# Kernel optimization log

Hardware: AMD Instinct MI355X
Metric: run time of the kernel (lower is better)

Reference implementation:

```python
import jax, jax.numpy as jnp
import numpy as np

TOP_K = 2

def setup_inputs() -> dict:
    key = jax.random.key(0)
    k1, k2, k3, k4 = jax.random.split(key, 4)
    T, H, I, E = 8192, 2048, 4096, 8
    s = 0.02
    return {
        "hidden_states": jax.random.normal(k1, (T, H), dtype=jnp.float32),
        "router_w": jax.random.normal(k2, (E, H), dtype=jnp.float32) * s,
        "ws": jax.random.normal(k3, (E, 2 * I, H), dtype=jnp.float32) * s,  # [gate; up]
        "w2s": jax.random.normal(k4, (E, H, I), dtype=jnp.float32) * s,
    }

def reference(hidden_states, router_w, ws, w2s):
    # Router gating: softmax over experts, top-k, NO renormalization
    logits = hidden_states @ router_w.T              # [T, E]
    probs = jax.nn.softmax(logits, axis=-1)
    topv, topi = jax.lax.top_k(probs, TOP_K)         # [T, K]
    T, E = probs.shape
    I = w2s.shape[2]
    # Dense routing-weight matrix [T, E]; top_k indices are unique per token
    w = jnp.zeros_like(probs).at[jnp.arange(T)[:, None], topi].set(topv)
    out = jnp.zeros_like(hidden_states)
    for e in range(E):  # fixed small expert loop; avoids [T,E,2I] blowup
        gate = hidden_states @ ws[e, :I].T           # [T, I]
        up = hidden_states @ ws[e, I:].T             # [T, I]
        h = jax.nn.silu(gate) * up                   # SwiGLU
        out = out + w[:, e:e + 1] * (h @ w2s[e].T)   # combine
    return out
```

## Files before the change

### kernel.cpp

```cpp
#include <hip/hip_runtime.h>
#include <cstdint>
#include <cstddef>

#define T_TOK 8192
#define HDIM  2048
#define IDIM  4096
#define NEXP  8
#define MAXT  72

typedef __bf16 bf16x8 __attribute__((ext_vector_type(8)));
typedef float  f32x4  __attribute__((ext_vector_type(4)));

#define BARRIER() __builtin_amdgcn_s_barrier()
#define LGKM0()   do { asm volatile("s_waitcnt lgkmcnt(0)" ::: "memory"); __builtin_amdgcn_sched_barrier(0); } while (0)
#define VMW(n)    do { asm volatile("s_waitcnt vmcnt(" #n ")" ::: "memory"); } while (0)
#define PRIO1()   __builtin_amdgcn_s_setprio(1)
#define PRIO0()   __builtin_amdgcn_s_setprio(0)

__device__ __forceinline__ unsigned short f2bf(float f) {
    union { float f; unsigned u; } v; v.f = f;
    unsigned r = v.u + 0x7FFFu + ((v.u >> 16) & 1u);
    return (unsigned short)(r >> 16);
}

__device__ __forceinline__ void gload16(const void* g, void* l) {
    __builtin_amdgcn_global_load_lds((__attribute__((address_space(1))) void*)g,
                                     (__attribute__((address_space(3))) void*)l,
                                     16, 0, 0);
}

__global__ __launch_bounds__(256) void router_k(const float* __restrict__ hs,
                                                const float* __restrict__ rw,
                                                float* __restrict__ wgt,
                                                int* __restrict__ counts,
                                                int* __restrict__ lists) {
    int gid  = blockIdx.x * 256 + threadIdx.x;
    int tok  = gid >> 6;
    int lane = threadIdx.x & 63;
    const float* x = hs + (size_t)tok * HDIM;

    float acc[NEXP];
#pragma unroll
    for (int e = 0; e < NEXP; ++e) acc[e] = 0.f;
    for (int h = lane; h < HDIM; h += 64) {
        float xv = x[h];
#pragma unroll
        for (int e = 0; e < NEXP; ++e) acc[e] = fmaf(xv, rw[e * HDIM + h], acc[e]);
    }
#pragma unroll
    for (int off = 32; off > 0; off >>= 1) {
#pragma unroll
        for (int e = 0; e < NEXP; ++e) acc[e] += __shfl_xor(acc[e], off, 64);
    }
    if (lane == 0) {
        float m = acc[0];
#pragma unroll
        for (int e = 1; e < NEXP; ++e) m = fmaxf(m, acc[e]);
        float p[NEXP]; float s = 0.f;
#pragma unroll
        for (int e = 0; e < NEXP; ++e) { p[e] = expf(acc[e] - m); s += p[e]; }
        float inv = 1.f / s;
        int i1 = 0;
#pragma unroll
        for (int e = 1; e < NEXP; ++e) if (acc[e] > acc[i1]) i1 = e;
        int i2 = -1;
#pragma unroll
        for (int e = 0; e < NEXP; ++e) if (e != i1 && (i2 < 0 || acc[e] > acc[i2])) i2 = e;
#pragma unroll
        for (int e = 0; e < NEXP; ++e)
            wgt[(size_t)tok * NEXP + e] = (e == i1 || e == i2) ? p[e] * inv : 0.f;
        int p1 = atomicAdd(&counts[i1], 1);
        lists[i1 * T_TOK + p1] = tok;
        int p2 = atomicAdd(&counts[i2], 1);
        lists[i2 * T_TOK + p2] = (1 << 16) | tok;
    }
}

__global__ void plan_k(const int* __restrict__ counts, int* __restrict__ offs,
                       int* __restrict__ desc, int* __restrict__ ntiles) {
    if (threadIdx.x == 0 && blockIdx.x == 0) {
        int off = 0, n = 0;
        for (int e = 0; e < NEXP; ++e) {
            offs[e] = off;
            int nt = (counts[e] + 255) >> 8;
            for (int t = 0; t < nt; ++t) desc[n++] = (e << 16) | t;
            off += nt * 256;
        }
        *ntiles = n;
    }
}

__global__ __launch_bounds__(256) void cvt_k(const float* __restrict__ in,
                                             unsigned short* __restrict__ out, long n4) {
    long i      = (long)blockIdx.x * 256 + threadIdx.x;
    long stride = (long)gridDim.x * 256;
    const float4* in4 = (const float4*)in;
    ushort4* out4 = (ushort4*)out;
    for (long j = i; j < n4; j += stride) {
        float4 v = in4[j];
        ushort4 o;
        o.x = f2bf(v.x); o.y = f2bf(v.y); o.z = f2bf(v.z); o.w = f2bf(v.w);
        out4[j] = o;
    }
}

__global__ __launch_bounds__(512, 2) void gemm1_k(const unsigned short* __restrict__ A,
                                                  const unsigned short* __restrict__ Wall,
                                                  unsigned short* __restrict__ Hout,
                                                  const int* __restrict__ lists,
                                                  const int* __restrict__ counts,
                                                  const int* __restrict__ offs,
                                                  const int* __restrict__ desc,
                                                  const int* __restrict__ ntiles) {
    const int slot = blockIdx.y;
    if (slot >= *ntiles) return;
    const int dsc = desc[slot];
    const int e = dsc >> 16, tt = dsc & 0xFFFF;
    const int cnt = counts[e];
    const int t0 = tt * 256;
    const int* list = lists + e * T_TOK;
    const unsigned short* W = Wall + (size_t)e * 2 * IDIM * HDIM;
    const int hbase = offs[e];
    const int n0 = blockIdx.x * 128;

    extern __shared__ __align__(16) char lds[];

    const int tid  = threadIdx.x;
    const int lane = tid & 63;
    const int wid  = tid >> 6;
    const int wr   = wid >> 2;
    const int wc   = wid & 3;

    const int prow = tid >> 3;
    const int pcol = (tid & 7) * 16;
    const int lcol = (pcol ^ ((prow & 7) << 4)) >> 1;
    unsigned aoff[4];
#pragma unroll
    for (int i = 0; i < 4; ++i) {
        int g = t0 + i * 64 + prow;
        int tok = list[(g < cnt) ? g : t0] & 0xFFFF;
        aoff[i] = (unsigned)tok * HDIM + lcol;
    }
    unsigned goff[2], uoff[2];
#pragma unroll
    for (int i = 0; i < 2; ++i) {
        goff[i] = (unsigned)(n0 + i * 64 + prow) * HDIM + lcol;
        uoff[i] = (unsigned)(IDIM + n0 + i * 64 + prow) * HDIM + lcol;
    }
    const int dst = tid * 16;

#define SG_AH0(b, t) do { unsigned k0_ = (unsigned)((t) & 31) * 64;      \
    gload16(A + aoff[0] + k0_, lds + (b) * 32768 + dst);                 \
    gload16(A + aoff[1] + k0_, lds + (b) * 32768 + 8192 + dst); } while (0)
#define SG_AH1(b, t) do { unsigned k0_ = (unsigned)((t) & 31) * 64;      \
    gload16(A + aoff[2] + k0_, lds + (b) * 32768 + 16384 + dst);         \
    gload16(A + aoff[3] + k0_, lds + (b) * 32768 + 24576 + dst); } while (0)
#define SG_G(b, t) do { unsigned k0_ = (unsigned)((t) & 31) * 64;        \
    gload16(W + goff[0] + k0_, lds + 65536 + (b) * 16384 + dst);         \
    gload16(W + goff[1] + k0_, lds + 65536 + (b) * 16384 + 8192 + dst); } while (0)
#define SG_U(b, t) do { unsigned k0_ = (unsigned)((t) & 31) * 64;        \
    gload16(W + uoff[0] + k0_, lds + 98304 + (b) * 16384 + dst);         \
    gload16(W + uoff[1] + k0_, lds + 98304 + (b) * 16384 + 8192 + dst); } while (0)

    const int frd = (lane & 7) << 4;
    const int cb0 = (((lane >> 4) * 16)     ) ^ frd;
    const int cb1 = (((lane >> 4) * 16) | 64) ^ frd;
    const int arow = (wr * 64 + (lane & 15)) * 128;
    const int brow = (wc * 32 + (lane & 15)) * 128;

    f32x4 accg[8][2], accu[8][2];
#pragma unroll
    for (int mi = 0; mi < 8; ++mi)
#pragma unroll
        for (int ni = 0; ni < 2; ++ni) {
            accg[mi][ni] = (f32x4){0.f, 0.f, 0.f, 0.f};
            accu[mi][ni] = (f32x4){0.f, 0.f, 0.f, 0.f};
        }

    SG_AH0(0, 0); SG_G(0, 0); SG_U(0, 0); SG_AH1(0, 0);
    SG_AH0(1, 1); SG_G(1, 1);
    VMW(0);
    BARRIER();

    const int NT = HDIM / 64;
    for (int kt = 0; kt < NT; ++kt) {
        const int b  = kt & 1;
        const int bn = b ^ 1;
        const char* la = lds + b * 32768 + arow;
        const char* lg = lds + 65536 + b * 16384 + brow;
        const char* lu = lds + 98304 + b * 16384 + brow;
        bf16x8 a0[2][4], bg[2][2], bu[2][2];

#pragma unroll
        for (int mi = 0; mi < 4; ++mi) {
            a0[0][mi] = *(const bf16x8*)(la + mi * 2048 + cb0);
            a0[1][mi] = *(const bf16x8*)(la + mi * 2048 + cb1);
        }
#pragma unroll
        for (int ni = 0; ni < 2; ++ni) {
            bg[0][ni] = *(const bf16x8*)(lg + ni * 2048 + cb0);
            bg[1][ni] = *(const bf16x8*)(lg + ni * 2048 + cb1);
        }
        SG_AH1(bn, kt + 1);
        BARRIER(); LGKM0(); PRIO1();
#pragma unroll
        for (int ks = 0; ks < 2; ++ks)
#pragma unroll
            for (int mi = 0; mi < 4; ++mi)
#pragma unroll
                for (int ni = 0; ni < 2; ++ni)
                    accg[mi][ni] = __builtin_amdgcn_mfma_f32_16x16x32_bf16(a0[ks][mi], bg[ks][ni], accg[mi][ni], 0, 0, 0);
        PRIO0();
        VMW(6);
        BARRIER();

#pragma unroll
        for (int ni = 0; ni < 2; ++ni) {
            bu[0][ni] = *(const bf16x8*)(lu + ni * 2048 + cb0);
            bu[1][ni] = *(const bf16x8*)(lu + ni * 2048 + cb1);
        }
        SG_U(bn, kt + 1);
        BARRIER(); LGKM0(); PRIO1();
#pragma unroll
        for (int ks = 0; ks < 2; ++ks)
#pragma unroll
            for (int mi = 0; mi < 4; ++mi)
#pragma unroll
                for (int ni = 0; ni < 2; ++ni)
                    accu[mi][ni] = __builtin_amdgcn_mfma_f32_16x16x32_bf16(a0[ks][mi], bu[ks][ni], accu[mi][ni], 0, 0, 0);
        PRIO0(); BARRIER();

#pragma unroll
        for (int mi = 0; mi < 4; ++mi) {
            a0[0][mi] = *(const bf16x8*)(la + 16384 + mi * 2048 + cb0);
            a0[1][mi] = *(const bf16x8*)(la + 16384 + mi * 2048 + cb1);
        }
        SG_AH0(b, kt + 2);
        BARRIER(); LGKM0(); PRIO1();
#pragma unroll
        for (int ks = 0; ks < 2; ++ks)
#pragma unroll
            for (int mi = 0; mi < 4; ++mi)
#pragma unroll
                for (int ni = 0; ni < 2; ++ni)
                    accg[mi + 4][ni] = __builtin_amdgcn_mfma_f32_16x16x32_bf16(a0[ks][mi], bg[ks][ni], accg[mi + 4][ni], 0, 0, 0);
        PRIO0(); BARRIER();

        SG_G(b, kt + 2);
        PRIO1();
#pragma unroll
        for (int ks = 0; ks < 2; ++ks)
#pragma unroll
            for (int mi = 0; mi < 4; ++mi)
#pragma unroll
                for (int ni = 0; ni < 2; ++ni)
                    accu[mi + 4][ni] = __builtin_amdgcn_mfma_f32_16x16x32_bf16(a0[ks][mi], bu[ks][ni], accu[mi + 4][ni], 0, 0, 0);
        PRIO0();
        VMW(8);
        BARRIER();
    }
    VMW(0);
#undef SG_AH0
#undef SG_AH1
#undef SG_G
#undef SG_U

#pragma unroll
    for (int mi = 0; mi < 8; ++mi)
#pragma unroll
        for (int ni = 0; ni < 2; ++ni)
#pragma unroll
            for (int j = 0; j < 4; ++j) {
                int qr = mi >> 2, m = mi & 3;
                int row = hbase + t0 + qr * 128 + wr * 64 + m * 16 + ((lane >> 4) << 2) + j;
                int col = n0 + wc * 32 + ni * 16 + (lane & 15);
                float g = accg[mi][ni][j], u = accu[mi][ni][j];
                float hv = (g / (1.f + expf(-g))) * u;
                Hout[(size_t)row * IDIM + col] = f2bf(hv);
            }
}

__global__ __launch_bounds__(512, 2) void gemm2_k(const unsigned short* __restrict__ Ah,
                                                  const unsigned short* __restrict__ Ball,
                                                  const float* __restrict__ wgt,
                                                  float* __restrict__ outP,
                                                  const int* __restrict__ lists,
                                                  const int* __restrict__ counts,
                                                  const int* __restrict__ offs,
                                                  const int* __restrict__ desc,
                                                  const int* __restrict__ ntiles) {
    const int slot = blockIdx.y;
    if (slot >= *ntiles) return;
    const int dsc = desc[slot];
    const int e = dsc >> 16, tt = dsc & 0xFFFF;
    const int cnt = counts[e];
    const int t0 = tt * 256;
    const int* list = lists + e * T_TOK;
    const unsigned short* B = Ball + (size_t)e * HDIM * IDIM;
    const int hbase = offs[e];
    const int n0 = blockIdx.x * 128;

    __shared__ __align__(16) char lds[98304];

    const int tid  = threadIdx.x;
    const int lane = tid & 63;
    const int wid  = tid >> 6;
    const int wr   = wid >> 2;
    const int wc   = wid & 3;

    const int prow = tid >> 3;
    const int pcol = (tid & 7) * 16;
    const int lcol = (pcol ^ ((prow & 7) << 4)) >> 1;
    unsigned aoff[4];
#pragma unroll
    for (int i = 0; i < 4; ++i)
        aoff[i] = (unsigned)(hbase + t0 + i * 64 + prow) * IDIM + lcol;
    unsigned boff[2];
#pragma unroll
    for (int i = 0; i < 2; ++i)
        boff[i] = (unsigned)(n0 + i * 64 + prow) * IDIM + lcol;
    const int dst = tid * 16;

#define SG_AH0(b, t) do { unsigned k0_ = (unsigned)((t) & 63) * 64;       \
    gload16(Ah + aoff[0] + k0_, lds + (b) * 32768 + dst);                 \
    gload16(Ah + aoff[1] + k0_, lds + (b) * 32768 + 8192 + dst); } while (0)
#define SG_AH1(b, t) do { unsigned k0_ = (unsigned)((t) & 63) * 64;       \
    gload16(Ah + aoff[2] + k0_, lds + (b) * 32768 + 16384 + dst);         \
    gload16(Ah + aoff[3] + k0_, lds + (b) * 32768 + 24576 + dst); } while (0)
#define SG_B(b, t) do { unsigned k0_ = (unsigned)((t) & 63) * 64;         \
    gload16(B + boff[0] + k0_, lds + 65536 + (b) * 16384 + dst);          \
    gload16(B + boff[1] + k0_, lds + 65536 + (b) * 16384 + 8192 + dst); } while (0)

    const int frd = (lane & 7) << 4;
    const int cb0 = (((lane >> 4) * 16)     ) ^ frd;
    const int cb1 = (((lane >> 4) * 16) | 64) ^ frd;
    const int arow = (wr * 64 + (lane & 15)) * 128;
    const int brow = (wc * 32 + (lane & 15)) * 128;

    f32x4 acc[8][2];
#pragma unroll
    for (int mi = 0; mi < 8; ++mi)
#pragma unroll
        for (int ni = 0; ni < 2; ++ni) acc[mi][ni] = (f32x4){0.f, 0.f, 0.f, 0.f};

    SG_AH0(0, 0); SG_B(0, 0); SG_AH1(0, 0);
    SG_AH0(1, 1);
    VMW(0);
    BARRIER();

    const int NT = IDIM / 64;
    for (int kt = 0; kt < NT; ++kt) {
        const int b  = kt & 1;
        const int bn = b ^ 1;
        const char* la = lds + b * 32768 + arow;
        const char* lb = lds + 65536 + b * 16384 + brow;
        bf16x8 a0[2][4], bb[2][2];

#pragma unroll
        for (int mi = 0; mi < 4; ++mi) {
            a0[0][mi] = *(const bf16x8*)(la + mi * 2048 + cb0);
            a0[1][mi] = *(const bf16x8*)(la + mi * 2048 + cb1);
        }
#pragma unroll
        for (int ni = 0; ni < 2; ++ni) {
            bb[0][ni] = *(const bf16x8*)(lb + ni * 2048 + cb0);
            bb[1][ni] = *(const bf16x8*)(lb + ni * 2048 + cb1);
        }
        SG_AH1(bn, kt + 1);
        SG_B(bn, kt + 1);
        BARRIER(); LGKM0(); PRIO1();
#pragma unroll
        for (int ks = 0; ks < 2; ++ks)
#pragma unroll
            for (int mi = 0; mi < 4; ++mi)
#pragma unroll
                for (int ni = 0; ni < 2; ++ni)
                    acc[mi][ni] = __builtin_amdgcn_mfma_f32_16x16x32_bf16(a0[ks][mi], bb[ks][ni], acc[mi][ni], 0, 0, 0);
        PRIO0(); BARRIER();

#pragma unroll
        for (int mi = 0; mi < 4; ++mi) {
            a0[0][mi] = *(const bf16x8*)(la + 16384 + mi * 2048 + cb0);
            a0[1][mi] = *(const bf16x8*)(la + 16384 + mi * 2048 + cb1);
        }
        SG_AH0(b, kt + 2);
        BARRIER(); LGKM0(); PRIO1();
#pragma unroll
        for (int ks = 0; ks < 2; ++ks)
#pragma unroll
            for (int mi = 0; mi < 4; ++mi)
#pragma unroll
                for (int ni = 0; ni < 2; ++ni)
                    acc[mi + 4][ni] = __builtin_amdgcn_mfma_f32_16x16x32_bf16(a0[ks][mi], bb[ks][ni], acc[mi + 4][ni], 0, 0, 0);
        PRIO0();
        VMW(2);
        BARRIER();
    }
    VMW(0);
#undef SG_AH0
#undef SG_AH1
#undef SG_B

#pragma unroll
    for (int mi = 0; mi < 8; ++mi) {
        int qr = mi >> 2, m = mi & 3;
#pragma unroll
        for (int j = 0; j < 4; ++j) {
            int row_l = qr * 128 + wr * 64 + m * 16 + ((lane >> 4) << 2) + j;
            int g = t0 + row_l;
            if (g < cnt) {
                int ent = list[g];
                int tok = ent & 0xFFFF;
                int sl  = ent >> 16;
                float w = wgt[(size_t)tok * NEXP + e];
                float* o = outP + (size_t)sl * T_TOK * HDIM + (size_t)tok * HDIM;
#pragma unroll
                for (int ni = 0; ni < 2; ++ni) {
                    int col = n0 + wc * 32 + ni * 16 + (lane & 15);
                    o[col] = w * acc[mi][ni][j];
                }
            }
        }
    }
}

__global__ __launch_bounds__(256) void combine_k(const float* __restrict__ p0,
                                                 const float* __restrict__ p1,
                                                 float* __restrict__ out, long n4) {
    long i      = (long)blockIdx.x * 256 + threadIdx.x;
    long stride = (long)gridDim.x * 256;
    const float4* a4 = (const float4*)p0;
    const float4* b4 = (const float4*)p1;
    float4* o4 = (float4*)out;
    for (long j = i; j < n4; j += stride) {
        float4 a = a4[j], b = b4[j];
        o4[j] = make_float4(a.x + b.x, a.y + b.y, a.z + b.z, a.w + b.w);
    }
}

extern "C" void kernel_launch(void* const* d_in, const int* in_sizes, int n_in,
                              void* d_out, int out_size, void* d_ws, size_t ws_size,
                              hipStream_t stream) {
    const float* hs  = (const float*)d_in[0];
    const float* rw  = (const float*)d_in[1];
    const float* ws  = (const float*)d_in[2];
    const float* w2s = (const float*)d_in[3];
    float* out = (float*)d_out;

    char* wsp = (char*)d_ws;
    unsigned short* hs_bf = (unsigned short*)(wsp);
    unsigned short* w_bf  = (unsigned short*)(wsp + 33554432ULL);
    unsigned short* w2_bf = (unsigned short*)(wsp + 301989888ULL);
    unsigned short* h_bf  = (unsigned short*)(wsp + 436207616ULL);
    float*          outP  = (float*)(wsp + 587202560ULL);
    float*          wgt   = (float*)(wsp + 721420288ULL);
    int*            counts = (int*)(wsp + 721682432ULL);
    int*            offs   = (int*)(wsp + 721682560ULL);
    int*            lists  = (int*)(wsp + 721682688ULL);
    int*            desc   = (int*)(wsp + 721944832ULL);
    int*            ntiles = (int*)(wsp + 721945344ULL);

    hipMemsetAsync(counts, 0, NEXP * sizeof(int), stream);
    cvt_k<<<2048, 256, 0, stream>>>(hs, hs_bf, (long)T_TOK * HDIM / 4);
    cvt_k<<<4096, 256, 0, stream>>>(ws, w_bf, (long)NEXP * 2 * IDIM * HDIM / 4);
    cvt_k<<<4096, 256, 0, stream>>>(w2s, w2_bf, (long)NEXP * HDIM * IDIM / 4);
    router_k<<<(T_TOK * 64) / 256, 256, 0, stream>>>(hs, rw, wgt, counts, lists);
    plan_k<<<1, 64, 0, stream>>>(counts, offs, desc, ntiles);

    gemm1_k<<<dim3(IDIM / 128, MAXT), 512, 131072, stream>>>(
        hs_bf, w_bf, h_bf, lists, counts, offs, desc, ntiles);
    gemm2_k<<<dim3(HDIM / 128, MAXT), 512, 0, stream>>>(
        h_bf, w2_bf, wgt, outP, lists, counts, offs, desc, ntiles);
    combine_k<<<2048, 256, 0, stream>>>(outP, outP + (size_t)T_TOK * HDIM, out,
                                        (long)T_TOK * HDIM / 4);
}
```

Measured before the change: 1.437 ms.

## Widen gemm2 output tile to 256 columns with split B staging

Doubles the N tile of the second expert GEMM from 128 to 256 columns. Each block now holds a 256x256 accumulator tile, and B is staged in two halves interleaved with the MFMA phases, so one A tile in LDS serves twice as many columns. LDS moves to 128KB of dynamic shared memory and accumulator registers double. That may lower occupancy under launch_bounds(512,2) and halves the grid's x dimension, so fewer blocks are available for parallelism.

```diff
diff --git a/kernel.cpp b/kernel.cpp
--- a/kernel.cpp
+++ b/kernel.cpp
@@ -298,9 +298,9 @@
     const int* list = lists + e * T_TOK;
     const unsigned short* B = Ball + (size_t)e * HDIM * IDIM;
     const int hbase = offs[e];
-    const int n0 = blockIdx.x * 128;
-
-    __shared__ __align__(16) char lds[98304];
+    const int n0 = blockIdx.x * 256;
+
+    extern __shared__ __align__(16) char lds[];
 
     const int tid  = threadIdx.x;
     const int lane = tid & 63;
@@ -311,14 +311,12 @@
     const int prow = tid >> 3;
     const int pcol = (tid & 7) * 16;
     const int lcol = (pcol ^ ((prow & 7) << 4)) >> 1;
-    unsigned aoff[4];
-#pragma unroll
-    for (int i = 0; i < 4; ++i)
+    unsigned aoff[4], boff[4];
+#pragma unroll
+    for (int i = 0; i < 4; ++i) {
         aoff[i] = (unsigned)(hbase + t0 + i * 64 + prow) * IDIM + lcol;
-    unsigned boff[2];
-#pragma unroll
-    for (int i = 0; i < 2; ++i)
         boff[i] = (unsigned)(n0 + i * 64 + prow) * IDIM + lcol;
+    }
     const int dst = tid * 16;
 
 #define SG_AH0(b, t) do { unsigned k0_ = (unsigned)((t) & 63) * 64;       \
@@ -327,24 +325,27 @@
 #define SG_AH1(b, t) do { unsigned k0_ = (unsigned)((t) & 63) * 64;       \
     gload16(Ah + aoff[2] + k0_, lds + (b) * 32768 + 16384 + dst);         \
     gload16(Ah + aoff[3] + k0_, lds + (b) * 32768 + 24576 + dst); } while (0)
-#define SG_B(b, t) do { unsigned k0_ = (unsigned)((t) & 63) * 64;         \
-    gload16(B + boff[0] + k0_, lds + 65536 + (b) * 16384 + dst);          \
-    gload16(B + boff[1] + k0_, lds + 65536 + (b) * 16384 + 8192 + dst); } while (0)
+#define SG_BH0(b, t) do { unsigned k0_ = (unsigned)((t) & 63) * 64;       \
+    gload16(B + boff[0] + k0_, lds + 65536 + (b) * 32768 + dst);          \
+    gload16(B + boff[1] + k0_, lds + 65536 + (b) * 32768 + 8192 + dst); } while (0)
+#define SG_BH1(b, t) do { unsigned k0_ = (unsigned)((t) & 63) * 64;       \
+    gload16(B + boff[2] + k0_, lds + 65536 + (b) * 32768 + 16384 + dst);  \
+    gload16(B + boff[3] + k0_, lds + 65536 + (b) * 32768 + 24576 + dst); } while (0)
 
     const int frd = (lane & 7) << 4;
     const int cb0 = (((lane >> 4) * 16)     ) ^ frd;
     const int cb1 = (((lane >> 4) * 16) | 64) ^ frd;
     const int arow = (wr * 64 + (lane & 15)) * 128;
-    const int brow = (wc * 32 + (lane & 15)) * 128;
-
-    f32x4 acc[8][2];
+    const int brow = (wc * 64 + (lane & 15)) * 128;
+
+    f32x4 acc[8][4];
 #pragma unroll
     for (int mi = 0; mi < 8; ++mi)
 #pragma unroll
-        for (int ni = 0; ni < 2; ++ni) acc[mi][ni] = (f32x4){0.f, 0.f, 0.f, 0.f};
-
-    SG_AH0(0, 0); SG_B(0, 0); SG_AH1(0, 0);
-    SG_AH0(1, 1);
+        for (int ni = 0; ni < 4; ++ni) acc[mi][ni] = (f32x4){0.f, 0.f, 0.f, 0.f};
+
+    SG_AH0(0, 0); SG_BH0(0, 0); SG_AH1(0, 0); SG_BH1(0, 0);
+    SG_AH0(1, 1); SG_BH0(1, 1);
     VMW(0);
     BARRIER();
 
@@ -353,8 +354,8 @@
         const int b  = kt & 1;
         const int bn = b ^ 1;
         const char* la = lds + b * 32768 + arow;
-        const char* lb = lds + 65536 + b * 16384 + brow;
-        bf16x8 a0[2][4], bb[2][2];
+        const char* lb = lds + 65536 + b * 32768 + brow;
+        bf16x8 a0[2][4], bb[2][4];
 
 #pragma unroll
         for (int mi = 0; mi < 4; ++mi) {
@@ -367,7 +368,6 @@
             bb[1][ni] = *(const bf16x8*)(lb + ni * 2048 + cb1);
         }
         SG_AH1(bn, kt + 1);
-        SG_B(bn, kt + 1);
         BARRIER(); LGKM0(); PRIO1();
 #pragma unroll
         for (int ks = 0; ks < 2; ++ks)
@@ -376,6 +376,22 @@
 #pragma unroll
                 for (int ni = 0; ni < 2; ++ni)
                     acc[mi][ni] = __builtin_amdgcn_mfma_f32_16x16x32_bf16(a0[ks][mi], bb[ks][ni], acc[mi][ni], 0, 0, 0);
+        PRIO0(); BARRIER();
+
+#pragma unroll
+        for (int ni = 0; ni < 2; ++ni) {
+            bb[0][ni + 2] = *(const bf16x8*)(lb + (ni + 2) * 2048 + cb0);
+            bb[1][ni + 2] = *(const bf16x8*)(lb + (ni + 2) * 2048 + cb1);
+        }
+        SG_BH1(bn, kt + 1);
+        BARRIER(); LGKM0(); PRIO1();
+#pragma unroll
+        for (int ks = 0; ks < 2; ++ks)
+#pragma unroll
+            for (int mi = 0; mi < 4; ++mi)
+#pragma unroll
+                for (int ni = 0; ni < 2; ++ni)
+                    acc[mi][ni + 2] = __builtin_amdgcn_mfma_f32_16x16x32_bf16(a0[ks][mi], bb[ks][ni + 2], acc[mi][ni + 2], 0, 0, 0);
         PRIO0(); BARRIER();
 
 #pragma unroll
@@ -392,22 +408,33 @@
 #pragma unroll
                 for (int ni = 0; ni < 2; ++ni)
                     acc[mi + 4][ni] = __builtin_amdgcn_mfma_f32_16x16x32_bf16(a0[ks][mi], bb[ks][ni], acc[mi + 4][ni], 0, 0, 0);
+        PRIO0(); BARRIER();
+
+        SG_BH0(b, kt + 2);
+        PRIO1();
+#pragma unroll
+        for (int ks = 0; ks < 2; ++ks)
+#pragma unroll
+            for (int mi = 0; mi < 4; ++mi)
+#pragma unroll
+                for (int ni = 0; ni < 2; ++ni)
+                    acc[mi + 4][ni + 2] = __builtin_amdgcn_mfma_f32_16x16x32_bf16(a0[ks][mi], bb[ks][ni + 2], acc[mi + 4][ni + 2], 0, 0, 0);
         PRIO0();
-        VMW(2);
+        VMW(4);
         BARRIER();
     }
     VMW(0);
 #undef SG_AH0
 #undef SG_AH1
-#undef SG_B
+#undef SG_BH0
+#undef SG_BH1
 
 #pragma unroll
     for (int mi = 0; mi < 8; ++mi) {
         int qr = mi >> 2, m = mi & 3;
 #pragma unroll
         for (int j = 0; j < 4; ++j) {
-            int row_l = qr * 128 + wr * 64 + m * 16 + ((lane >> 4) << 2) + j;
-            int g = t0 + row_l;
+            int g = t0 + qr * 128 + wr * 64 + m * 16 + ((lane >> 4) << 2) + j;
             if (g < cnt) {
                 int ent = list[g];
                 int tok = ent & 0xFFFF;
@@ -415,8 +442,8 @@
                 float w = wgt[(size_t)tok * NEXP + e];
                 float* o = outP + (size_t)sl * T_TOK * HDIM + (size_t)tok * HDIM;
 #pragma unroll
-                for (int ni = 0; ni < 2; ++ni) {
-                    int col = n0 + wc * 32 + ni * 16 + (lane & 15);
+                for (int ni = 0; ni < 4; ++ni) {
+                    int col = n0 + wc * 64 + ni * 16 + (lane & 15);
                     o[col] = w * acc[mi][ni][j];
                 }
             }
@@ -469,7 +496,7 @@
 
     gemm1_k<<<dim3(IDIM / 128, MAXT), 512, 131072, stream>>>(
         hs_bf, w_bf, h_bf, lists, counts, offs, desc, ntiles);
-    gemm2_k<<<dim3(HDIM / 128, MAXT), 512, 0, stream>>>(
+    gemm2_k<<<dim3(HDIM / 256, MAXT), 512, 131072, stream>>>(
         h_bf, w2_bf, wgt, outP, lists, counts, offs, desc, ntiles);
     combine_k<<<2048, 256, 0, stream>>>(outP, outP + (size_t)T_TOK * HDIM, out,
                                         (long)T_TOK * HDIM / 4);
```

Measured after the change: 1.377 ms. 1.04x faster.
